# Kernel tuning notes

Measured on AMD Instinct MI355X. Metric: run time of the kernel, lower is better.

The kernel has to match this reference:

```python
import jax, jax.numpy as jnp
import numpy as np

B, N = 256, 512
N_ITERS = 300      # FISTA iterations (fixed for jit)
POWER_ITERS = 30   # power iterations to estimate lambda_max(Q)


def setup_inputs():
    key = jax.random.key(0)
    k1, k2, k3 = jax.random.split(key, 3)
    rets = 0.1 * jax.random.normal(k1, (B, N), dtype=jnp.float32)
    covmat_sqrt = jax.random.normal(k2, (B, N, N), dtype=jnp.float32) / np.float32(np.sqrt(N))
    gamma = jax.random.uniform(k3, (B,), dtype=jnp.float32, minval=0.1, maxval=1.0)
    return {"rets": rets, "covmat_sqrt": covmat_sqrt, "gamma": gamma}


def project_simplex(v):
    # Row-wise Euclidean projection onto {w : w >= 0, sum(w) = 1} (Duchi et al. 2008).
    # With sum(w)=1 and w>=0, the bound w <= max_weight=1 is automatically satisfied.
    n = v.shape[-1]
    u = jnp.sort(v, axis=-1)[..., ::-1]          # descending
    css = jnp.cumsum(u, axis=-1)
    idx = jnp.arange(1, n + 1, dtype=v.dtype)
    rho = jnp.sum((u - (css - 1.0) / idx) > 0, axis=-1)            # [B], >= 1
    css_rho = jnp.take_along_axis(css, (rho - 1)[..., None], axis=-1)[..., 0]
    theta = (css_rho - 1.0) / rho.astype(v.dtype)
    return jnp.maximum(v - theta[..., None], 0.0)


def _solve(rets, covmat_sqrt, gamma):
    # Markowitz layer: maximize rets@w - ||(gamma*covmat_sqrt) @ w||^2
    #                  s.t. sum(w)=1, 0 <= w <= 1
    # == min_w  w^T Q w - rets^T w  over the probability simplex, Q = A^T A (PSD).
    A = gamma[:, None, None] * covmat_sqrt                  # [B,N,N]
    Q = jnp.einsum('bki,bkj->bij', A, A)                    # [B,N,N]

    # Lipschitz constant of gradient (2*lambda_max(Q)) via power iteration; no grads needed.
    Qs = jax.lax.stop_gradient(Q)
    v0 = jnp.full(rets.shape, 1.0 / np.sqrt(rets.shape[-1]), dtype=rets.dtype)
    def piter(v, _):
        v = jnp.einsum('bij,bj->bi', Qs, v)
        return v / (jnp.linalg.norm(v, axis=-1, keepdims=True) + 1e-12), None
    v, _ = jax.lax.scan(piter, v0, None, length=POWER_ITERS)
    lam = jnp.einsum('bi,bij,bj->b', v, Qs, v)              # lambda_max(Q) per sample
    eta = 1.0 / (2.0 * lam + 1e-8)                          # [B] step sizes

    # FISTA (accelerated projected gradient) on the simplex.
    w0 = jnp.full(rets.shape, 1.0 / rets.shape[-1], dtype=rets.dtype)
    t0 = jnp.asarray(1.0, dtype=rets.dtype)
    def step(carry, _):
        w, y, t = carry
        g = 2.0 * jnp.einsum('bij,bj->bi', Q, y) - rets
        w_new = project_simplex(y - eta[:, None] * g)
        t_new = 0.5 * (1.0 + jnp.sqrt(1.0 + 4.0 * t * t))
        y_new = w_new + ((t - 1.0) / t_new) * (w_new - w)
        return (w_new, y_new, t_new), None
    (w, _, _), _ = jax.lax.scan(step, (w0, w0, t0), None, length=N_ITERS)
    return w


def reference(rets, covmat_sqrt, gamma):
    return _solve(rets, covmat_sqrt, gamma)
```

## Files before the change

kernel.cpp:

```cpp
#include <hip/hip_runtime.h>
#include <hip/hip_fp16.h>

namespace {
constexpr int kN = 512;
constexpr int kB = 256;
constexpr int kPowerIters = 30;
constexpr int kFistaIters = 300;
constexpr int kCacheRows = 120;
}

typedef __attribute__((ext_vector_type(8))) short bf16x8;
typedef __attribute__((ext_vector_type(4))) float f32x4;

__device__ ushort g_Ct[(size_t)kB * kN * kN];
__device__ __half g_Q16[(size_t)kB * kN * kN];
__device__ unsigned int g_Q8[(size_t)kB * kN * kN / 4];

__device__ __forceinline__ float wave_sum64(float x) {
  x += __shfl_xor(x, 32, 64);
  x += __shfl_xor(x, 16, 64);
  x += __int_as_float(__builtin_amdgcn_update_dpp(0, __float_as_int(x), 0x128, 0xF, 0xF, true));
  x += __int_as_float(__builtin_amdgcn_ds_swizzle(__float_as_int(x), 0x101F));
  x += __int_as_float(__builtin_amdgcn_update_dpp(0, __float_as_int(x), 0x4E, 0xF, 0xF, true));
  x += __int_as_float(__builtin_amdgcn_update_dpp(0, __float_as_int(x), 0xB1, 0xF, 0xF, true));
  return x;
}
__device__ __forceinline__ float wave_max64(float x) {
  x = fmaxf(x, __shfl_xor(x, 32, 64));
  x = fmaxf(x, __shfl_xor(x, 16, 64));
  x = fmaxf(x, __int_as_float(__builtin_amdgcn_update_dpp(0, __float_as_int(x), 0x128, 0xF, 0xF, true)));
  x = fmaxf(x, __int_as_float(__builtin_amdgcn_ds_swizzle(__float_as_int(x), 0x101F)));
  x = fmaxf(x, __int_as_float(__builtin_amdgcn_update_dpp(0, __float_as_int(x), 0x4E, 0xF, 0xF, true)));
  x = fmaxf(x, __int_as_float(__builtin_amdgcn_update_dpp(0, __float_as_int(x), 0xB1, 0xF, 0xF, true)));
  return x;
}


__device__ __forceinline__ ushort f32_to_bf16(float f) {
  unsigned int u = __float_as_uint(f);
  unsigned int r = u + 0x7FFFu + ((u >> 16) & 1u);
  return (ushort)(r >> 16);
}

__global__ __launch_bounds__(256) void transpose_kernel(const float* __restrict__ C) {
  __shared__ ushort Ts[64][68];
  const int b = blockIdx.y;
  const int tk = blockIdx.x >> 3, ti = blockIdx.x & 7;
  const int k0 = tk * 64, i0 = ti * 64;
  const float* Cb = C + (size_t)b * kN * kN;
  ushort* Ct = g_Ct + (size_t)b * kN * kN;
  const int t = threadIdx.x;
  const int cq = t & 15;
  const int r0 = t >> 4;
#pragma unroll
  for (int p = 0; p < 4; ++p) {
    const int r = r0 + 16 * p;
    const float4 v = *(const float4*)(Cb + (size_t)(k0 + r) * kN + i0 + 4 * cq);
    ushort4 h;
    h.x = f32_to_bf16(v.x); h.y = f32_to_bf16(v.y);
    h.z = f32_to_bf16(v.z); h.w = f32_to_bf16(v.w);
    *(ushort4*)(&Ts[r][4 * cq]) = h;
  }
  __syncthreads();
#pragma unroll
  for (int p = 0; p < 4; ++p) {
    const int r = r0 + 16 * p;
    ushort4 h;
    h.x = Ts[4 * cq + 0][r];
    h.y = Ts[4 * cq + 1][r];
    h.z = Ts[4 * cq + 2][r];
    h.w = Ts[4 * cq + 3][r];
    *(ushort4*)(Ct + (size_t)(i0 + r) * kN + k0 + 4 * cq) = h;
  }
}


__global__ __launch_bounds__(256) void build_q_kernel(const float* __restrict__ gamma) {
  __shared__ ushort As[128][40];
  __shared__ ushort Bs[128][40];
  const int b = blockIdx.y;
  const int ti = blockIdx.x >> 2, tj = blockIdx.x & 3;
  const int i0 = ti * 128, j0 = tj * 128;
  const ushort* Ct = g_Ct + (size_t)b * kN * kN;
  const float gg = gamma[b];
  const float g2 = gg * gg;
  const int t = threadIdx.x;
  const int lane = t & 63, w = t >> 6;
  const int wr = w >> 1, wc = w & 1;
  const int m = lane & 15, q = lane >> 4;
  const int sr = t >> 2;
  const int ss = t & 3;

  f32x4 acc[4][4];
#pragma unroll
  for (int g = 0; g < 4; ++g)
#pragma unroll
    for (int h = 0; h < 4; ++h) acc[g][h] = (f32x4){0.f, 0.f, 0.f, 0.f};

  for (int k0 = 0; k0 < kN; k0 += 32) {
    const int4 a0 = *(const int4*)(Ct + (size_t)(i0 + sr) * kN + k0 + 8 * ss);
    const int4 a1 = *(const int4*)(Ct + (size_t)(i0 + sr + 64) * kN + k0 + 8 * ss);
    const int4 b0 = *(const int4*)(Ct + (size_t)(j0 + sr) * kN + k0 + 8 * ss);
    const int4 b1 = *(const int4*)(Ct + (size_t)(j0 + sr + 64) * kN + k0 + 8 * ss);
    __syncthreads();
    *(int4*)(&As[sr][8 * ss]) = a0;
    *(int4*)(&As[sr + 64][8 * ss]) = a1;
    *(int4*)(&Bs[sr][8 * ss]) = b0;
    *(int4*)(&Bs[sr + 64][8 * ss]) = b1;
    __syncthreads();
    bf16x8 fa[4], fb[4];
#pragma unroll
    for (int g = 0; g < 4; ++g)
      fa[g] = *(const bf16x8*)(&As[64 * wr + 16 * g + m][8 * q]);
#pragma unroll
    for (int h = 0; h < 4; ++h)
      fb[h] = *(const bf16x8*)(&Bs[64 * wc + 16 * h + m][8 * q]);
#pragma unroll
    for (int g = 0; g < 4; ++g)
#pragma unroll
      for (int h = 0; h < 4; ++h)
        acc[g][h] = __builtin_amdgcn_mfma_f32_16x16x32_bf16(fa[g], fb[h], acc[g][h], 0, 0, 0);
  }

  __half* Qb = g_Q16 + (size_t)b * kN * kN;
  unsigned char* q8b = (unsigned char*)g_Q8 + (size_t)b * kN * kN;
#pragma unroll
  for (int g = 0; g < 4; ++g) {
#pragma unroll
    for (int h = 0; h < 4; ++h) {
      const int col = j0 + 64 * wc + 16 * h + m;
      const int rbase = i0 + 64 * wr + 16 * g + 4 * q;
#pragma unroll
      for (int r = 0; r < 4; ++r)
        Qb[(size_t)(rbase + r) * kN + col] = __float2half(acc[g][h][r] * g2);
      unsigned int pk = 0;
      pk = __builtin_amdgcn_cvt_pk_fp8_f32(acc[g][h][0], acc[g][h][1], pk, false);
      pk = __builtin_amdgcn_cvt_pk_fp8_f32(acc[g][h][2], acc[g][h][3], pk, true);
      *(unsigned int*)(q8b + (size_t)col * kN + rbase) = pk;
    }
  }
}


__device__ __forceinline__ void fma8(const int4 raw, const float yj, float* acc) {
  const __half2* h2 = reinterpret_cast<const __half2*>(&raw);
#pragma unroll
  for (int k = 0; k < 4; ++k) {
    const float2 f = __half22float2(h2[k]);
    acc[2 * k]     = fmaf(f.x, yj, acc[2 * k]);
    acc[2 * k + 1] = fmaf(f.y, yj, acc[2 * k + 1]);
  }
}

__device__ __forceinline__ int fista_proj_update(const float z8[8], float w8[8], float y8[8],
                                                 float& tf, float& theta_io,
                                                 float* yv_s, short* yi_s,
                                                 unsigned long long m8_out[8],
                                                 float& dmax_out) {
  const int lane = threadIdx.x & 63;
  float theta = theta_io;
  int prev = -1;
  for (int r = 0; r < 60; ++r) {
    float ss = 0.f, cc = 0.f;
#pragma unroll
    for (int c = 0; c < 8; ++c)
      if (z8[c] > theta) { ss += z8[c]; cc += 1.0f; }
    ss = wave_sum64(ss);
    cc = wave_sum64(cc);
    const int cnt = (int)(cc + 0.5f);
    if (cnt == 0) {
      float s = 0.f;
#pragma unroll
      for (int c = 0; c < 8; ++c) s += z8[c];
      s = wave_sum64(s);
      theta = (s - 1.0f) * (1.0f / 512.0f);
      prev = -1;
      continue;
    }
    if (cnt == prev) break;
    theta = (ss - 1.0f) / cc;
    prev = cnt;
  }
  theta_io = theta;

  const float t_new = 0.5f * (1.0f + sqrtf(1.0f + 4.0f * tf * tf));
  const float coef = (tf - 1.0f) / t_new;
  tf = t_new;
  float yn8[8];
  float dmax = 0.f;
#pragma unroll
  for (int c = 0; c < 8; ++c) {
    const float wn = fmaxf(z8[c] - theta, 0.0f);
    const float yn = wn + coef * (wn - w8[c]);
    dmax = fmaxf(dmax, fmaxf(fabsf(wn - w8[c]), fabsf(yn - y8[c])));
    w8[c] = wn;
    y8[c] = yn;
    yn8[c] = yn;
  }
#pragma unroll
  for (int c = 0; c < 8; ++c) m8_out[c] = __ballot(yn8[c] != 0.0f);
  int base = 0;
  const unsigned long long lt = (1ull << lane) - 1ull;
#pragma unroll
  for (int c = 0; c < 8; ++c) {
    if (yn8[c] != 0.0f) {
      const int pos = base + __popcll(m8_out[c] & lt);
      yi_s[pos] = (short)(8 * lane + c);
      yv_s[pos] = yn8[c];
    }
    base += __popcll(m8_out[c]);
  }
  dmax_out = wave_max64(dmax);
  return base;
}


__global__ __launch_bounds__(1024) void solver_kernel(const float* __restrict__ rets,
                                                      float* __restrict__ out) {
  __shared__ __align__(16) ushort rowcache[kCacheRows][kN];
  __shared__ __align__(16) float yv_s[kN];
  __shared__ __align__(16) float zred_s[kN];
  __shared__ short yi_s[kN];
  __shared__ short cachedrow_s[kCacheRows];
  __shared__ float red_s[8];
  __shared__ int nact_s;
  __shared__ int done_s;

  const int t = threadIdx.x;
  const int lane = t & 63;
  const int w = t >> 6;
  const int b = blockIdx.x;
  const int4* Q16v = (const int4*)(g_Q16 + (size_t)b * kN * kN);
  const uint2* Q8v = (const uint2*)g_Q8 + (size_t)b * (kN * kN / 8);
  float* partial = reinterpret_cast<float*>(&rowcache[0][0]);

  if (t < kN) yv_s[t] = 0.044194173824159216f;
  if (t == 0) done_s = 0;
  __syncthreads();

  float invn = 1.0f;
  for (int it = 0; it < kPowerIters; ++it) {
    float acc[8] = {0.f, 0.f, 0.f, 0.f, 0.f, 0.f, 0.f, 0.f};
#pragma unroll 8
    for (int k = w; k < kN; k += 16) {
      const uint2 raw = Q8v[(size_t)k * 64 + lane];
      const float yj = yv_s[k];
      acc[0] = fmaf(__builtin_amdgcn_cvt_f32_fp8(raw.x, 0), yj, acc[0]);
      acc[1] = fmaf(__builtin_amdgcn_cvt_f32_fp8(raw.x, 1), yj, acc[1]);
      acc[2] = fmaf(__builtin_amdgcn_cvt_f32_fp8(raw.x, 2), yj, acc[2]);
      acc[3] = fmaf(__builtin_amdgcn_cvt_f32_fp8(raw.x, 3), yj, acc[3]);
      acc[4] = fmaf(__builtin_amdgcn_cvt_f32_fp8(raw.y, 0), yj, acc[4]);
      acc[5] = fmaf(__builtin_amdgcn_cvt_f32_fp8(raw.y, 1), yj, acc[5]);
      acc[6] = fmaf(__builtin_amdgcn_cvt_f32_fp8(raw.y, 2), yj, acc[6]);
      acc[7] = fmaf(__builtin_amdgcn_cvt_f32_fp8(raw.y, 3), yj, acc[7]);
    }
    float4* pp = (float4*)&partial[(w << 9) + (lane << 3)];
    pp[0] = make_float4(acc[0] * invn, acc[1] * invn, acc[2] * invn, acc[3] * invn);
    pp[1] = make_float4(acc[4] * invn, acc[5] * invn, acc[6] * invn, acc[7] * invn);
    __syncthreads();
    if (t < kN) {
      float u = 0.f;
#pragma unroll
      for (int ww = 0; ww < 16; ++ww) u += partial[(ww << 9) + t];
      yv_s[t] = u;
      const float qq = wave_sum64(u * u);
      if (lane == 0) red_s[w] = qq;
    }
    __syncthreads();
    float n2 = 0.f;
#pragma unroll
    for (int i = 0; i < 8; ++i) n2 += red_s[i];
    invn = 1.0f / (sqrtf(n2) + 1e-12f);
  }

  float eta;
  {
    float acc[8] = {0.f, 0.f, 0.f, 0.f, 0.f, 0.f, 0.f, 0.f};
#pragma unroll 8
    for (int k = w; k < kN; k += 16) {
      const int4 raw = Q16v[(size_t)k * 64 + lane];
      fma8(raw, yv_s[k], acc);
    }
    float4* pp = (float4*)&partial[(w << 9) + (lane << 3)];
    pp[0] = make_float4(acc[0] * invn, acc[1] * invn, acc[2] * invn, acc[3] * invn);
    pp[1] = make_float4(acc[4] * invn, acc[5] * invn, acc[6] * invn, acc[7] * invn);
    __syncthreads();
    if (t < kN) {
      float u = 0.f;
#pragma unroll
      for (int ww = 0; ww < 16; ++ww) u += partial[(ww << 9) + t];
      const float vt = yv_s[t] * invn;
      const float ql = wave_sum64(vt * u);
      if (lane == 0) red_s[w] = ql;
    }
    __syncthreads();
    float lam = 0.f;
#pragma unroll
    for (int i = 0; i < 8; ++i) lam += red_s[i];
    eta = 1.0f / (2.0f * 1.06f * lam + 1e-8f);
  }

  float w8[8], y8[8], r8[8];
  float tf = 1.0f;
  float theta_w = 0.0f;
  unsigned long long m8_prev[8] = {0, 0, 0, 0, 0, 0, 0, 0};
  if (t < kN) { yv_s[t] = 1.0f / 512.0f; yi_s[t] = (short)t; }
  if (t == 0) nact_s = kN;
  if (w == 0) {
    const float4 ra = *(const float4*)(rets + (size_t)b * kN + 8 * lane);
    const float4 rc = *(const float4*)(rets + (size_t)b * kN + 8 * lane + 4);
    r8[0] = ra.x; r8[1] = ra.y; r8[2] = ra.z; r8[3] = ra.w;
    r8[4] = rc.x; r8[5] = rc.y; r8[6] = rc.z; r8[7] = rc.w;
#pragma unroll
    for (int c = 0; c < 8; ++c) { w8[c] = 1.0f / 512.0f; y8[c] = 1.0f / 512.0f; }
  }
  __syncthreads();

  int it = 0;
  for (; it < kFistaIters; ++it) {
    const int na = nact_s;
    if (na <= kCacheRows || done_s) break;
    float acc[8] = {0.f, 0.f, 0.f, 0.f, 0.f, 0.f, 0.f, 0.f};
#pragma unroll 8
    for (int k = w; k < na; k += 16) {
      const int row = yi_s[k];
      fma8(Q16v[(size_t)row * 64 + lane], yv_s[k], acc);
    }
    float4* pp = (float4*)&partial[(w << 9) + (lane << 3)];
    pp[0] = make_float4(acc[0], acc[1], acc[2], acc[3]);
    pp[1] = make_float4(acc[4], acc[5], acc[6], acc[7]);
    __syncthreads();
    if (t < kN) {
      float u = 0.f;
#pragma unroll
      for (int ww = 0; ww < 16; ++ww) u += partial[(ww << 9) + t];
      zred_s[t] = u;
    }
    __syncthreads();
    if (w == 0) {
      float z8[8];
      const float4 za = *(const float4*)&zred_s[8 * lane];
      const float4 zb = *(const float4*)&zred_s[8 * lane + 4];
      z8[0] = y8[0] - eta * (2.0f * za.x - r8[0]);
      z8[1] = y8[1] - eta * (2.0f * za.y - r8[1]);
      z8[2] = y8[2] - eta * (2.0f * za.z - r8[2]);
      z8[3] = y8[3] - eta * (2.0f * za.w - r8[3]);
      z8[4] = y8[4] - eta * (2.0f * zb.x - r8[4]);
      z8[5] = y8[5] - eta * (2.0f * zb.y - r8[5]);
      z8[6] = y8[6] - eta * (2.0f * zb.z - r8[6]);
      z8[7] = y8[7] - eta * (2.0f * zb.w - r8[7]);
      float dmax;
      const int nb = fista_proj_update(z8, w8, y8, tf, theta_w, yv_s, yi_s, m8_prev, dmax);
      if (lane == 0) {
        nact_s = nb;
        if (dmax < 1e-7f) done_s = 1;
      }
    }
    __syncthreads();
  }

  const bool finished = (done_s != 0) || (it >= kFistaIters);
  if (!finished) {
    const int naf = nact_s;
    for (int k = w; k < naf; k += 16)
      *(int4*)(&rowcache[k][8 * lane]) = Q16v[(size_t)yi_s[k] * 64 + lane];
    if (t < kCacheRows) cachedrow_s[t] = (t < naf) ? yi_s[t] : (short)-1;
    __syncthreads();
  }
  if (w != 0) return;

  if (!finished) {
    int na = nact_s;
    bool cache_match = true;
    for (; it < kFistaIters; ++it) {
      float acc[8] = {0.f, 0.f, 0.f, 0.f, 0.f, 0.f, 0.f, 0.f};
      const int lim = na < kCacheRows ? na : kCacheRows;

      int P = lim;
      if (!cache_match) {
        for (int k0 = 0; k0 < lim; k0 += 64) {
          const int k = k0 + lane;
          const bool mis = (k < lim) && (cachedrow_s[k] != yi_s[k]);
          const unsigned long long mm = __ballot(mis);
          if (mm) { P = k0 + (int)__ffsll(mm) - 1; break; }
        }
      }

#pragma unroll 8
      for (int k = 0; k < P; ++k)
        fma8(*(const int4*)(&rowcache[k][8 * lane]), yv_s[k], acc);
      for (int k = P; k < lim; ++k) {
        const int row = yi_s[k];
        const int4 raw = Q16v[(size_t)row * 64 + lane];
        *(int4*)(&rowcache[k][8 * lane]) = raw;
        if (lane == 0) cachedrow_s[k] = (short)row;
        fma8(raw, yv_s[k], acc);
      }
#pragma unroll 4
      for (int k = lim; k < na; ++k) {
        const int row = yi_s[k];
        fma8(Q16v[(size_t)row * 64 + lane], yv_s[k], acc);
      }

      float z8[8];
#pragma unroll
      for (int c = 0; c < 8; ++c)
        z8[c] = y8[c] - eta * (2.0f * acc[c] - r8[c]);

      float dmax;
      unsigned long long m8[8];
      na = fista_proj_update(z8, w8, y8, tf, theta_w, yv_s, yi_s, m8, dmax);
      bool same = true;
#pragma unroll
      for (int c = 0; c < 8; ++c) { same = same && (m8[c] == m8_prev[c]); m8_prev[c] = m8[c]; }
      cache_match = same;
      if (dmax < 1e-7f) break;
    }
  }

  *(float4*)(out + (size_t)b * kN + 8 * lane)     = make_float4(w8[0], w8[1], w8[2], w8[3]);
  *(float4*)(out + (size_t)b * kN + 8 * lane + 4) = make_float4(w8[4], w8[5], w8[6], w8[7]);
}

extern "C" void kernel_launch(void* const* d_in, const int* in_sizes, int n_in,
                              void* d_out, int out_size, void* d_ws, size_t ws_size,
                              hipStream_t stream) {
  (void)in_sizes; (void)n_in; (void)out_size; (void)d_ws; (void)ws_size;
  const float* rets  = (const float*)d_in[0];
  const float* cov   = (const float*)d_in[1];
  const float* gamma = (const float*)d_in[2];
  float* out = (float*)d_out;

  transpose_kernel<<<dim3(64, kB), 256, 0, stream>>>(cov);
  build_q_kernel<<<dim3(16, kB), 256, 0, stream>>>(gamma);
  solver_kernel<<<kB, 1024, 0, stream>>>(rets, out);
}
```

Baseline: 1.433 ms.

## Split sparse-phase FISTA matvec across four waves with shared-memory flag sync

The sparse tail of the FISTA loop, which ran on a single wave, now uses four waves. Each wave takes every fourth active row, reading it from the LDS row cache or from global memory and refilling the cache per row on a mismatch. Waves 1-3 write partial sums to shared memory and signal through volatile progress flags. Wave 0 reduces the partials, runs the simplex projection and publishes the new active set. This cuts the serial latency of the per-iteration matvec at the cost of spin-wait synchronisation and extra LDS traffic. The prefix-based cache-match scan is replaced by a per-row tag check.

```diff
diff --git a/kernel.cpp b/kernel.cpp
--- a/kernel.cpp
+++ b/kernel.cpp
@@ -155,7 +155,6 @@
 __device__ __forceinline__ int fista_proj_update(const float z8[8], float w8[8], float y8[8],
                                                  float& tf, float& theta_io,
                                                  float* yv_s, short* yi_s,
-                                                 unsigned long long m8_out[8],
                                                  float& dmax_out) {
   const int lane = threadIdx.x & 63;
   float theta = theta_io;
@@ -187,6 +186,7 @@
   const float coef = (tf - 1.0f) / t_new;
   tf = t_new;
   float yn8[8];
+  unsigned long long m8[8];
   float dmax = 0.f;
 #pragma unroll
   for (int c = 0; c < 8; ++c) {
@@ -198,17 +198,17 @@
     yn8[c] = yn;
   }
 #pragma unroll
-  for (int c = 0; c < 8; ++c) m8_out[c] = __ballot(yn8[c] != 0.0f);
+  for (int c = 0; c < 8; ++c) m8[c] = __ballot(yn8[c] != 0.0f);
   int base = 0;
   const unsigned long long lt = (1ull << lane) - 1ull;
 #pragma unroll
   for (int c = 0; c < 8; ++c) {
     if (yn8[c] != 0.0f) {
-      const int pos = base + __popcll(m8_out[c] & lt);
+      const int pos = base + __popcll(m8[c] & lt);
       yi_s[pos] = (short)(8 * lane + c);
       yv_s[pos] = yn8[c];
     }
-    base += __popcll(m8_out[c]);
+    base += __popcll(m8[c]);
   }
   dmax_out = wave_max64(dmax);
   return base;
@@ -220,9 +220,11 @@
   __shared__ __align__(16) ushort rowcache[kCacheRows][kN];
   __shared__ __align__(16) float yv_s[kN];
   __shared__ __align__(16) float zred_s[kN];
+  __shared__ __align__(16) float partB_s[3 * kN];
   __shared__ short yi_s[kN];
   __shared__ short cachedrow_s[kCacheRows];
   __shared__ float red_s[8];
+  __shared__ int prog_s[4];
   __shared__ int nact_s;
   __shared__ int done_s;
 
@@ -236,6 +238,7 @@
 
   if (t < kN) yv_s[t] = 0.044194173824159216f;
   if (t == 0) done_s = 0;
+  if (t < 4) prog_s[t] = -1;
   __syncthreads();
 
   float invn = 1.0f;
@@ -303,7 +306,6 @@
   float w8[8], y8[8], r8[8];
   float tf = 1.0f;
   float theta_w = 0.0f;
-  unsigned long long m8_prev[8] = {0, 0, 0, 0, 0, 0, 0, 0};
   if (t < kN) { yv_s[t] = 1.0f / 512.0f; yi_s[t] = (short)t; }
   if (t == 0) nact_s = kN;
   if (w == 0) {
@@ -350,7 +352,7 @@
       z8[6] = y8[6] - eta * (2.0f * zb.z - r8[6]);
       z8[7] = y8[7] - eta * (2.0f * zb.w - r8[7]);
       float dmax;
-      const int nb = fista_proj_update(z8, w8, y8, tf, theta_w, yv_s, yi_s, m8_prev, dmax);
+      const int nb = fista_proj_update(z8, w8, y8, tf, theta_w, yv_s, yi_s, dmax);
       if (lane == 0) {
         nact_s = nb;
         if (dmax < 1e-7f) done_s = 1;
@@ -367,56 +369,74 @@
     if (t < kCacheRows) cachedrow_s[t] = (t < naf) ? yi_s[t] : (short)-1;
     __syncthreads();
   }
-  if (w != 0) return;
+  if (w >= 4) return;
 
   if (!finished) {
+    volatile int* prog = (volatile int*)prog_s;
     int na = nact_s;
-    bool cache_match = true;
     for (; it < kFistaIters; ++it) {
       float acc[8] = {0.f, 0.f, 0.f, 0.f, 0.f, 0.f, 0.f, 0.f};
-      const int lim = na < kCacheRows ? na : kCacheRows;
-
-      int P = lim;
-      if (!cache_match) {
-        for (int k0 = 0; k0 < lim; k0 += 64) {
-          const int k = k0 + lane;
-          const bool mis = (k < lim) && (cachedrow_s[k] != yi_s[k]);
-          const unsigned long long mm = __ballot(mis);
-          if (mm) { P = k0 + (int)__ffsll(mm) - 1; break; }
+      for (int k = w; k < na; k += 4) {
+        const int row = yi_s[k];
+        int4 raw;
+        if (k < kCacheRows && cachedrow_s[k] == (short)row) {
+          raw = *(const int4*)(&rowcache[k][8 * lane]);
+        } else {
+          raw = Q16v[(size_t)row * 64 + lane];
+          if (k < kCacheRows) {
+            *(int4*)(&rowcache[k][8 * lane]) = raw;
+            if (lane == 0) cachedrow_s[k] = (short)row;
+          }
         }
-      }
-
-#pragma unroll 8
-      for (int k = 0; k < P; ++k)
-        fma8(*(const int4*)(&rowcache[k][8 * lane]), yv_s[k], acc);
-      for (int k = P; k < lim; ++k) {
-        const int row = yi_s[k];
-        const int4 raw = Q16v[(size_t)row * 64 + lane];
-        *(int4*)(&rowcache[k][8 * lane]) = raw;
-        if (lane == 0) cachedrow_s[k] = (short)row;
         fma8(raw, yv_s[k], acc);
       }
-#pragma unroll 4
-      for (int k = lim; k < na; ++k) {
-        const int row = yi_s[k];
-        fma8(Q16v[(size_t)row * 64 + lane], yv_s[k], acc);
+
+      if (w != 0) {
+        float4* pp = (float4*)&partB_s[((w - 1) << 9) + (lane << 3)];
+        pp[0] = make_float4(acc[0], acc[1], acc[2], acc[3]);
+        pp[1] = make_float4(acc[4], acc[5], acc[6], acc[7]);
+        __threadfence_block();
+        if (lane == 0) prog[w] = it;
+        while (prog[0] < it) __builtin_amdgcn_s_sleep(1);
+        __threadfence_block();
+        na = nact_s;
+        if (done_s) break;
+      } else {
+        while (prog[1] < it || prog[2] < it || prog[3] < it)
+          __builtin_amdgcn_s_sleep(1);
+        __threadfence_block();
+        float z8[8];
+        const float4* p1 = (const float4*)&partB_s[(0 << 9) + (lane << 3)];
+        const float4* p2 = (const float4*)&partB_s[(1 << 9) + (lane << 3)];
+        const float4* p3 = (const float4*)&partB_s[(2 << 9) + (lane << 3)];
+        const float4 a1 = p1[0], b1 = p1[1];
+        const float4 a2 = p2[0], b2 = p2[1];
+        const float4 a3 = p3[0], b3 = p3[1];
+        float u8[8];
+        u8[0] = acc[0] + a1.x + a2.x + a3.x;
+        u8[1] = acc[1] + a1.y + a2.y + a3.y;
+        u8[2] = acc[2] + a1.z + a2.z + a3.z;
+        u8[3] = acc[3] + a1.w + a2.w + a3.w;
+        u8[4] = acc[4] + b1.x + b2.x + b3.x;
+        u8[5] = acc[5] + b1.y + b2.y + b3.y;
+        u8[6] = acc[6] + b1.z + b2.z + b3.z;
+        u8[7] = acc[7] + b1.w + b2.w + b3.w;
+#pragma unroll
+        for (int c = 0; c < 8; ++c)
+          z8[c] = y8[c] - eta * (2.0f * u8[c] - r8[c]);
+
+        float dmax;
+        const int nb = fista_proj_update(z8, w8, y8, tf, theta_w, yv_s, yi_s, dmax);
+        const bool dn = (dmax < 1e-7f);
+        if (lane == 0) { nact_s = nb; done_s = dn ? 1 : 0; }
+        __threadfence_block();
+        if (lane == 0) prog[0] = it;
+        na = nb;
+        if (dn) break;
       }
-
-      float z8[8];
-#pragma unroll
-      for (int c = 0; c < 8; ++c)
-        z8[c] = y8[c] - eta * (2.0f * acc[c] - r8[c]);
-
-      float dmax;
-      unsigned long long m8[8];
-      na = fista_proj_update(z8, w8, y8, tf, theta_w, yv_s, yi_s, m8, dmax);
-      bool same = true;
-#pragma unroll
-      for (int c = 0; c < 8; ++c) { same = same && (m8[c] == m8_prev[c]); m8_prev[c] = m8[c]; }
-      cache_match = same;
-      if (dmax < 1e-7f) break;
-    }
-  }
+    }
+  }
+  if (w != 0) return;
 
   *(float4*)(out + (size_t)b * kN + 8 * lane)     = make_float4(w8[0], w8[1], w8[2], w8[3]);
   *(float4*)(out + (size_t)b * kN + 8 * lane + 4) = make_float4(w8[4], w8[5], w8[6], w8[7]);
```

Measured after the change: 1.500 ms. 1.05x slower.
